# Kernel optimization log

Hardware: AMD Instinct MI355X
Metric: run time of the kernel (lower is better)

The kernel has to match this reference:

```python
import jax, jax.numpy as jnp
import numpy as np

B, N, H, DH, CZ = 1, 768, 16, 32, 128
D = H * DH  # 512
EPS = 1e-5


def layer_norm(x, w, b):
    mu = jnp.mean(x, axis=-1, keepdims=True)
    var = jnp.var(x, axis=-1, keepdims=True)
    return (x - mu) * jax.lax.rsqrt(var + EPS) * w + b


def setup_inputs() -> dict:
    key = jax.random.key(0)
    ks = jax.random.split(key, 10)
    sc = 0.02
    return {
        "s": jax.random.normal(ks[0], (B, N, D), jnp.float32),
        "z": jax.random.normal(ks[1], (B, N, N, CZ), jnp.float32),
        "norm_s_w": jnp.ones((D,), jnp.float32),
        "norm_s_b": jnp.zeros((D,), jnp.float32),
        "q_w": jax.random.normal(ks[2], (D, D), jnp.float32) * sc,
        "q_b": jax.random.normal(ks[3], (D,), jnp.float32) * sc,
        "k_w": jax.random.normal(ks[4], (D, D), jnp.float32) * sc,
        "v_w": jax.random.normal(ks[5], (D, D), jnp.float32) * sc,
        "g_w": jax.random.normal(ks[6], (D, D), jnp.float32) * sc,
        "zn_w": jnp.ones((CZ,), jnp.float32),
        "zn_b": jnp.zeros((CZ,), jnp.float32),
        "z_w": jax.random.normal(ks[7], (CZ, H), jnp.float32) * sc,
        "o_w": jax.random.normal(ks[8], (D, D), jnp.float32) * sc,
    }


def reference(s, z, norm_s_w, norm_s_b, q_w, q_b, k_w, v_w, g_w, zn_w, zn_b, z_w, o_w):
    # initial_norm on s
    s_n = layer_norm(s, norm_s_w, norm_s_b)
    # QKV projections (q has bias, k/v do not)
    q = (s_n @ q_w + q_b).reshape(B, N, H, DH)
    k = (s_n @ k_w).reshape(B, N, H, DH)
    v = (s_n @ v_w).reshape(B, N, H, DH)
    # attention scores [B, H, N, N]
    scores = jnp.einsum("bihd,bjhd->bhij", q, k) * (DH ** -0.5)
    # pair bias: layernorm(z) then linear c_z -> H, permute to [B, H, N, N]
    z_bias = layer_norm(z, zn_w, zn_b) @ z_w            # [B, N, N, H]
    z_bias = jnp.transpose(z_bias, (0, 3, 1, 2))         # [B, H, N, N]
    a = jax.nn.softmax(scores + z_bias, axis=-1)
    # attend
    o = jnp.einsum("bhij,bjhd->bihd", a, v).reshape(B, N, D)
    # sigmoid gate from normed s
    g = jax.nn.sigmoid(s_n @ g_w)
    # output projection
    return (o * g) @ o_w
```

## Files before the change

kernel.cpp:

```cpp
#include <hip/hip_runtime.h>
#include <hip/hip_bf16.h>

typedef float f32x4 __attribute__((ext_vector_type(4)));
typedef short bf16x8 __attribute__((ext_vector_type(8)));
typedef unsigned short u16;

#define NTOK 768
#define DMOD 512
#define NH   16
#define DH   32
#define CZd  128
#define NN   (768*768)

static __device__ __forceinline__ u16 f2bf(float f) {
  __hip_bfloat16 h = __float2bfloat16(f);
  return __builtin_bit_cast(u16, h);
}
static __device__ __forceinline__ float bf2f(u16 u) {
  unsigned int x = ((unsigned int)u) << 16;
  return __builtin_bit_cast(float, x);
}

__global__ __launch_bounds__(256) void prep_kernel(
    const float* __restrict__ s, const float* __restrict__ nsw, const float* __restrict__ nsb,
    const float* __restrict__ qw, const float* __restrict__ kw, const float* __restrict__ vw,
    const float* __restrict__ gw, const float* __restrict__ ow,
    const float* __restrict__ z, const float* __restrict__ znw, const float* __restrict__ znb,
    const float* __restrict__ zwp,
    u16* __restrict__ wbf, u16* __restrict__ snb, u16* __restrict__ biasb) {
  __shared__ char SM[18432];
  int bid = blockIdx.x;
  int t = threadIdx.x;

  if (bid < 1280) {
    float (*tbuf)[33] = (float(*)[33])SM;
    int seg = bid / 256;
    int tile = bid % 256;
    int k0 = (tile / 16) * 32;
    int n0 = (tile % 16) * 32;
    const float* src = seg==0?qw: seg==1?kw: seg==2?vw: seg==3?gw: ow;
    u16* out = wbf + (size_t)seg * (DMOD*DMOD);
    int tr  = t / 8;
    int tc4 = (t % 8) * 4;
    float4 v = *(const float4*)(src + (size_t)(k0+tr)*DMOD + n0 + tc4);
    tbuf[tr][tc4+0]=v.x; tbuf[tr][tc4+1]=v.y; tbuf[tr][tc4+2]=v.z; tbuf[tr][tc4+3]=v.w;
    __syncthreads();
    int nr  = t / 8;
    int kc4 = (t % 8) * 4;
    ushort4 o;
    o.x = f2bf(tbuf[kc4+0][nr]);
    o.y = f2bf(tbuf[kc4+1][nr]);
    o.z = f2bf(tbuf[kc4+2][nr]);
    o.w = f2bf(tbuf[kc4+3][nr]);
    *(ushort4*)(out + (size_t)(n0+nr)*DMOD + k0 + kc4) = o;
    return;
  }

  if (bid < 1472) {
    int i = (bid - 1280)*4 + (t >> 6);
    int lane = t & 63;
    const float* row = s + (size_t)i*DMOD + lane*8;
    float4 a0 = *(const float4*)(row);
    float4 a1 = *(const float4*)(row + 4);
    float sum = a0.x+a0.y+a0.z+a0.w + a1.x+a1.y+a1.z+a1.w;
    float sq  = a0.x*a0.x+a0.y*a0.y+a0.z*a0.z+a0.w*a0.w
              + a1.x*a1.x+a1.y*a1.y+a1.z*a1.z+a1.w*a1.w;
    #pragma unroll
    for (int mk=1; mk<64; mk<<=1) { sum += __shfl_xor(sum,mk); sq += __shfl_xor(sq,mk); }
    float mu  = sum * (1.f/512.f);
    float var = sq  * (1.f/512.f) - mu*mu;
    float rs  = rsqrtf(var + 1e-5f);
    float4 w0 = *(const float4*)(nsw + lane*8);
    float4 w1 = *(const float4*)(nsw + lane*8 + 4);
    float4 b0 = *(const float4*)(nsb + lane*8);
    float4 b1 = *(const float4*)(nsb + lane*8 + 4);
    bf16x8 o;
    o[0]=(short)f2bf((a0.x-mu)*rs*w0.x+b0.x);
    o[1]=(short)f2bf((a0.y-mu)*rs*w0.y+b0.y);
    o[2]=(short)f2bf((a0.z-mu)*rs*w0.z+b0.z);
    o[3]=(short)f2bf((a0.w-mu)*rs*w0.w+b0.w);
    o[4]=(short)f2bf((a1.x-mu)*rs*w1.x+b1.x);
    o[5]=(short)f2bf((a1.y-mu)*rs*w1.y+b1.y);
    o[6]=(short)f2bf((a1.z-mu)*rs*w1.z+b1.z);
    o[7]=(short)f2bf((a1.w-mu)*rs*w1.w+b1.w);
    *(bf16x8*)(snb + (size_t)i*DMOD + lane*8) = o;
    return;
  }

  u16*   zt   = (u16*)SM;
  float* znws = (float*)(SM + 17408);
  float* znbs = (float*)(SM + 17920);
  int zb = bid - 1472;
  int i = zb / 12, j0 = (zb % 12) * 64;
  int lane = t & 63, wv = t >> 6;
  int c16 = lane & 15, c4 = lane >> 4;
  if (t < 128) znws[t] = znw[t];
  else znbs[t-128] = znb[t-128];
  int rsub = t >> 5;
  int ch4  = (t & 31) * 4;
  const float* ztile = z + ((size_t)i*NTOK + j0)*CZd;
  float4 xv[8];
  #pragma unroll
  for (int it=0; it<8; it++)
    xv[it] = *(const float4*)(ztile + (size_t)(it*8 + rsub)*CZd + ch4);
  bf16x8 bfr[4];
  #pragma unroll
  for (int ks=0; ks<4; ks++) {
    #pragma unroll
    for (int jj=0; jj<8; jj++)
      bfr[ks][jj] = (short)f2bf(zwp[(ks*32 + c4*8 + jj)*16 + c16]);
  }
  float mu8[8], rs8[8];
  #pragma unroll
  for (int it=0; it<8; it++) {
    float4 v = xv[it];
    float sum = v.x+v.y+v.z+v.w;
    float sq  = v.x*v.x+v.y*v.y+v.z*v.z+v.w*v.w;
    #pragma unroll
    for (int mk=1; mk<32; mk<<=1) { sum += __shfl_xor(sum,mk); sq += __shfl_xor(sq,mk); }
    float mu = sum*(1.f/128.f);
    mu8[it] = mu;
    rs8[it] = rsqrtf(sq*(1.f/128.f) - mu*mu + 1e-5f);
  }
  __syncthreads();
  float4 w4 = *(const float4*)(znws + ch4);
  float4 b4 = *(const float4*)(znbs + ch4);
  #pragma unroll
  for (int it=0; it<8; it++) {
    float4 v = xv[it];
    float mu = mu8[it], rs = rs8[it];
    ushort4 o;
    o.x = f2bf((v.x-mu)*rs*w4.x + b4.x);
    o.y = f2bf((v.y-mu)*rs*w4.y + b4.y);
    o.z = f2bf((v.z-mu)*rs*w4.z + b4.z);
    o.w = f2bf((v.w-mu)*rs*w4.w + b4.w);
    *(ushort4*)(zt + (it*8 + rsub)*136 + ch4) = o;
  }
  __syncthreads();
  f32x4 acc = {0,0,0,0};
  #pragma unroll
  for (int ks=0; ks<4; ks++) {
    bf16x8 af = *(const bf16x8*)(zt + (wv*16 + c16)*136 + ks*32 + c4*8);
    acc = __builtin_amdgcn_mfma_f32_16x16x32_bf16(af, bfr[ks], acc, 0,0,0);
  }
  int jl = j0 + wv*16 + c4*4;
  u16* bp = biasb + (size_t)c16*NN + (size_t)i*NTOK + jl;
  ushort4 st;
  st.x = f2bf(acc[0]); st.y = f2bf(acc[1]); st.z = f2bf(acc[2]); st.w = f2bf(acc[3]);
  *(ushort4*)bp = st;
}

__global__ __launch_bounds__(256) void qkvg_kernel(
    const u16* __restrict__ sn, const u16* __restrict__ wts, const float* __restrict__ qb,
    u16* __restrict__ qo, u16* __restrict__ ko, u16* __restrict__ vTo, float* __restrict__ go) {
  __shared__ u16 As[32*40];
  __shared__ u16 Bs[64*40];
  int bid = blockIdx.x;
  int mb = bid % 24, nb = bid / 24;
  int wsel = nb >> 3, n0 = (nb & 7) * 64, m0 = mb * 32;
  const u16* wt = wts + (size_t)wsel * (DMOD*DMOD);
  int t = threadIdx.x, lane = t & 63, wv = t >> 6;
  int wm = (wv >> 1) * 16, wn = (wv & 1) * 32;
  int c16 = lane & 15, c4 = lane >> 4;
  int sr = t >> 2, sc = t & 3;
  f32x4 acc0={0,0,0,0}, acc1={0,0,0,0};
  for (int k0 = 0; k0 < DMOD; k0 += 32) {
    bf16x8 av;
    if (t < 128) av = *(const bf16x8*)(sn + (size_t)(m0+sr)*DMOD + k0 + sc*8);
    bf16x8 bv = *(const bf16x8*)(wt + (size_t)(n0+sr)*DMOD + k0 + sc*8);
    __syncthreads();
    if (t < 128) *(bf16x8*)(As + sr*40 + sc*8) = av;
    *(bf16x8*)(Bs + sr*40 + sc*8) = bv;
    __syncthreads();
    bf16x8 a  = *(const bf16x8*)(As + (wm + c16)*40      + c4*8);
    bf16x8 b0 = *(const bf16x8*)(Bs + (wn + c16)*40      + c4*8);
    bf16x8 b1 = *(const bf16x8*)(Bs + (wn + 16 + c16)*40 + c4*8);
    acc0 = __builtin_amdgcn_mfma_f32_16x16x32_bf16(a,b0,acc0,0,0,0);
    acc1 = __builtin_amdgcn_mfma_f32_16x16x32_bf16(a,b1,acc1,0,0,0);
  }
  int r0 = c4*4;
  #pragma unroll
  for (int bn=0; bn<2; bn++) {
    f32x4 acc = bn==0?acc0:acc1;
    #pragma unroll
    for (int rr=0; rr<4; rr++) {
      int i = m0 + wm + r0 + rr;
      int n = n0 + wn + bn*16 + c16;
      float val = acc[rr];
      if (wsel == 0)      { val += qb[n]; qo[(size_t)i*DMOD + n] = f2bf(val); }
      else if (wsel == 1) { ko[(size_t)i*DMOD + n] = f2bf(val); }
      else if (wsel == 2) { vTo[(size_t)n*NTOK + i] = f2bf(val); }
      else                { go[(size_t)i*DMOD + n] = 1.f/(1.f + expf(-val)); }
    }
  }
}

__global__ __launch_bounds__(256) void attn_kernel(
    const u16* __restrict__ qm, const u16* __restrict__ km, const u16* __restrict__ vTm,
    const u16* __restrict__ bias, const float* __restrict__ gm, u16* __restrict__ og) {
  __shared__ u16 Bt[4][16*72];
  __shared__ u16 Pt[4][16*72];
  __shared__ float OS[4][16][33];
  __shared__ float LS[4][16];
  int h  = blockIdx.x & 15;
  int i0 = (blockIdx.x >> 4) * 16;
  int t = threadIdx.x, lane = t & 63, wv = t >> 6;
  int c16 = lane & 15, c4 = lane >> 4, r0 = c4 * 4;
  bf16x8 qf = *(const bf16x8*)(qm + (size_t)(i0 + c16)*DMOD + h*DH + c4*8);
  f32x4 o0 = {0,0,0,0}, o1 = {0,0,0,0};
  float ls[4] = {0.f,0.f,0.f,0.f};
  const float scale = 0.17677669529663687f;
  const u16* bbase = bias + (size_t)h*NN + (size_t)i0*NTOK;
  int br = lane >> 3;
  int bc = (lane & 7) * 8;
  u16* bt = &Bt[wv][0];
  u16* pt = &Pt[wv][0];
  for (int jj = 0; jj < 3; jj++) {
    int j0 = wv*192 + jj*64;
    bf16x8 bv0 = *(const bf16x8*)(bbase + (size_t)br*NTOK     + j0 + bc);
    bf16x8 bv1 = *(const bf16x8*)(bbase + (size_t)(br+8)*NTOK + j0 + bc);
    bf16x8 kf0 = *(const bf16x8*)(km + (size_t)(j0 +  0 + c16)*DMOD + h*DH + c4*8);
    bf16x8 kf1 = *(const bf16x8*)(km + (size_t)(j0 + 16 + c16)*DMOD + h*DH + c4*8);
    bf16x8 kf2 = *(const bf16x8*)(km + (size_t)(j0 + 32 + c16)*DMOD + h*DH + c4*8);
    bf16x8 kf3 = *(const bf16x8*)(km + (size_t)(j0 + 48 + c16)*DMOD + h*DH + c4*8);
    *(bf16x8*)(bt + br*72 + bc)     = bv0;
    *(bf16x8*)(bt + (br+8)*72 + bc) = bv1;
    f32x4 zz = {0,0,0,0};
    f32x4 s0 = __builtin_amdgcn_mfma_f32_16x16x32_bf16(qf,kf0,zz,0,0,0);
    f32x4 s1 = __builtin_amdgcn_mfma_f32_16x16x32_bf16(qf,kf1,zz,0,0,0);
    f32x4 s2 = __builtin_amdgcn_mfma_f32_16x16x32_bf16(qf,kf2,zz,0,0,0);
    f32x4 s3 = __builtin_amdgcn_mfma_f32_16x16x32_bf16(qf,kf3,zz,0,0,0);
    #pragma unroll
    for (int rr=0; rr<4; rr++) {
      int row = (r0 + rr) * 72;
      float p0 = __expf(s0[rr]*scale + bf2f(bt[row + 0*16 + c16]));
      float p1 = __expf(s1[rr]*scale + bf2f(bt[row + 1*16 + c16]));
      float p2 = __expf(s2[rr]*scale + bf2f(bt[row + 2*16 + c16]));
      float p3 = __expf(s3[rr]*scale + bf2f(bt[row + 3*16 + c16]));
      ls[rr] += p0 + p1 + p2 + p3;
      pt[row + 0*16 + c16] = f2bf(p0);
      pt[row + 1*16 + c16] = f2bf(p1);
      pt[row + 2*16 + c16] = f2bf(p2);
      pt[row + 3*16 + c16] = f2bf(p3);
    }
    #pragma unroll
    for (int ks=0; ks<2; ks++) {
      bf16x8 pf = *(const bf16x8*)(pt + c16*72 + ks*32 + c4*8);
      bf16x8 v0 = *(const bf16x8*)(vTm + (size_t)(h*DH + c16)*NTOK      + j0 + ks*32 + c4*8);
      bf16x8 v1 = *(const bf16x8*)(vTm + (size_t)(h*DH + 16 + c16)*NTOK + j0 + ks*32 + c4*8);
      o0 = __builtin_amdgcn_mfma_f32_16x16x32_bf16(pf, v0, o0, 0,0,0);
      o1 = __builtin_amdgcn_mfma_f32_16x16x32_bf16(pf, v1, o1, 0,0,0);
    }
  }
  #pragma unroll
  for (int rr=0; rr<4; rr++) {
    float l = ls[rr];
    l += __shfl_xor(l,1); l += __shfl_xor(l,2); l += __shfl_xor(l,4); l += __shfl_xor(l,8);
    OS[wv][r0+rr][c16]      = o0[rr];
    OS[wv][r0+rr][16 + c16] = o1[rr];
    if (c16 == 0) LS[wv][r0+rr] = l;
  }
  __syncthreads();
  #pragma unroll
  for (int u=0; u<2; u++) {
    int idx = t + u*256;
    int row = idx >> 5, d = idx & 31;
    float osum = OS[0][row][d] + OS[1][row][d] + OS[2][row][d] + OS[3][row][d];
    float lsum = LS[0][row] + LS[1][row] + LS[2][row] + LS[3][row];
    int i = i0 + row;
    float g = gm[(size_t)i*DMOD + h*DH + d];
    og[(size_t)i*DMOD + h*DH + d] = f2bf(osum/lsum*g);
  }
}

__global__ __launch_bounds__(256) void out_kernel(
    const u16* __restrict__ og, const u16* __restrict__ owT, float* __restrict__ out) {
  __shared__ u16 As[32*40];
  __shared__ u16 Bs[64*40];
  int bid = blockIdx.x;
  int mb = bid % 24, nb = bid / 24;
  int m0 = mb*32, n0 = nb*64;
  int t = threadIdx.x, lane = t & 63, wv = t >> 6;
  int wm = (wv >> 1) * 16, wn = (wv & 1) * 32;
  int c16 = lane & 15, c4 = lane >> 4;
  int sr = t >> 2, sc = t & 3;
  f32x4 acc0={0,0,0,0}, acc1={0,0,0,0};
  for (int k0 = 0; k0 < DMOD; k0 += 32) {
    bf16x8 av;
    if (t < 128) av = *(const bf16x8*)(og + (size_t)(m0+sr)*DMOD + k0 + sc*8);
    bf16x8 bv = *(const bf16x8*)(owT + (size_t)(n0+sr)*DMOD + k0 + sc*8);
    __syncthreads();
    if (t < 128) *(bf16x8*)(As + sr*40 + sc*8) = av;
    *(bf16x8*)(Bs + sr*40 + sc*8) = bv;
    __syncthreads();
    bf16x8 a  = *(const bf16x8*)(As + (wm + c16)*40      + c4*8);
    bf16x8 b0 = *(const bf16x8*)(Bs + (wn + c16)*40      + c4*8);
    bf16x8 b1 = *(const bf16x8*)(Bs + (wn + 16 + c16)*40 + c4*8);
    acc0 = __builtin_amdgcn_mfma_f32_16x16x32_bf16(a,b0,acc0,0,0,0);
    acc1 = __builtin_amdgcn_mfma_f32_16x16x32_bf16(a,b1,acc1,0,0,0);
  }
  int r0 = c4*4;
  #pragma unroll
  for (int bn=0; bn<2; bn++) {
    f32x4 acc = bn==0?acc0:acc1;
    #pragma unroll
    for (int rr=0; rr<4; rr++)
      out[(size_t)(m0 + wm + r0 + rr)*DMOD + n0 + wn + bn*16 + c16] = acc[rr];
  }
}

extern "C" void kernel_launch(void* const* d_in, const int* in_sizes, int n_in,
                              void* d_out, int out_size, void* d_ws, size_t ws_size,
                              hipStream_t stream) {
  const float* s   = (const float*)d_in[0];
  const float* z   = (const float*)d_in[1];
  const float* nsw = (const float*)d_in[2];
  const float* nsb = (const float*)d_in[3];
  const float* qw  = (const float*)d_in[4];
  const float* qb  = (const float*)d_in[5];
  const float* kw  = (const float*)d_in[6];
  const float* vw  = (const float*)d_in[7];
  const float* gw  = (const float*)d_in[8];
  const float* znw = (const float*)d_in[9];
  const float* znb = (const float*)d_in[10];
  const float* zw  = (const float*)d_in[11];
  const float* ow  = (const float*)d_in[12];
  float* out = (float*)d_out;

  char* p = (char*)d_ws;
  u16* w_bf    = (u16*)p;  p += (size_t)5*DMOD*DMOD*2;
  u16* sn_bf   = (u16*)p;  p += (size_t)NTOK*DMOD*2;
  u16* q_bf    = (u16*)p;  p += (size_t)NTOK*DMOD*2;
  u16* k_bf    = (u16*)p;  p += (size_t)NTOK*DMOD*2;
  u16* vT_bf   = (u16*)p;  p += (size_t)NTOK*DMOD*2;
  float* g_f   = (float*)p; p += (size_t)NTOK*DMOD*4;
  u16* og_bf   = (u16*)p;  p += (size_t)NTOK*DMOD*2;
  u16* bias_bf = (u16*)p;  p += (size_t)NH*NN*2;

  prep_kernel<<<dim3(10688), dim3(256), 0, stream>>>(
      s, nsw, nsb, qw, kw, vw, gw, ow, z, znw, znb, zw, w_bf, sn_bf, bias_bf);
  qkvg_kernel<<<dim3(768), dim3(256), 0, stream>>>(sn_bf, w_bf, qb, q_bf, k_bf, vT_bf, g_f);
  attn_kernel<<<dim3(768), dim3(256), 0, stream>>>(q_bf, k_bf, vT_bf, bias_bf, g_f, og_bf);
  out_kernel<<<dim3(192), dim3(256), 0, stream>>>(og_bf, w_bf + (size_t)4*DMOD*DMOD, out);
}
```

Before: 101.1 us.

## Split z-bias prep kernel, relayout bias as [i,h,j], drop LDS staging in GEMMs

Splits the prep kernel in two. A small kernel pretransposes z_w to bf16, and a separate zprep kernel normalizes z with per-row 8-lane reductions and wider loads. The pair-bias buffer is reordered to [i][h][j], and the attention kernel now reads bias straight from global memory instead of staging it in LDS. The QKVG and output GEMMs drop shared-memory tiling and barriers and load MFMA fragments directly from global memory with unrolling. This trades LDS traffic and syncs for more global and L2 traffic, and adds one extra kernel launch.

```diff
diff --git a/kernel.cpp b/kernel.cpp
--- a/kernel.cpp
+++ b/kernel.cpp
@@ -21,19 +21,16 @@
   return __builtin_bit_cast(float, x);
 }
 
-__global__ __launch_bounds__(256) void prep_kernel(
+__global__ __launch_bounds__(256) void pre_kernel(
     const float* __restrict__ s, const float* __restrict__ nsw, const float* __restrict__ nsb,
     const float* __restrict__ qw, const float* __restrict__ kw, const float* __restrict__ vw,
-    const float* __restrict__ gw, const float* __restrict__ ow,
-    const float* __restrict__ z, const float* __restrict__ znw, const float* __restrict__ znb,
-    const float* __restrict__ zwp,
-    u16* __restrict__ wbf, u16* __restrict__ snb, u16* __restrict__ biasb) {
-  __shared__ char SM[18432];
+    const float* __restrict__ gw, const float* __restrict__ ow, const float* __restrict__ zwp,
+    u16* __restrict__ wbf, u16* __restrict__ snb, u16* __restrict__ zwT) {
   int bid = blockIdx.x;
   int t = threadIdx.x;
 
   if (bid < 1280) {
-    float (*tbuf)[33] = (float(*)[33])SM;
+    __shared__ float tbuf[32][33];
     int seg = bid / 256;
     int tile = bid % 256;
     int k0 = (tile / 16) * 32;
@@ -87,54 +84,73 @@
     return;
   }
 
-  u16*   zt   = (u16*)SM;
-  float* znws = (float*)(SM + 17408);
-  float* znbs = (float*)(SM + 17920);
-  int zb = bid - 1472;
-  int i = zb / 12, j0 = (zb % 12) * 64;
-  int lane = t & 63, wv = t >> 6;
+  #pragma unroll
+  for (int e=0; e<8; e++) {
+    int idx = t*8 + e;
+    int n = idx >> 7, k = idx & 127;
+    zwT[idx] = f2bf(zwp[k*16 + n]);
+  }
+}
+
+__global__ __launch_bounds__(256) void zprep_kernel(
+    const float* __restrict__ z, const float* __restrict__ znw, const float* __restrict__ znb,
+    const u16* __restrict__ zwT, u16* __restrict__ biasb) {
+  __shared__ u16 zt[64*136];
+  int bid = blockIdx.x;
+  int i = bid / 12, j0 = (bid % 12) * 64;
+  int t = threadIdx.x, lane = t & 63, wv = t >> 6;
   int c16 = lane & 15, c4 = lane >> 4;
-  if (t < 128) znws[t] = znw[t];
-  else znbs[t-128] = znb[t-128];
-  int rsub = t >> 5;
-  int ch4  = (t & 31) * 4;
+  int rsub = lane >> 3;
+  int ch0  = (lane & 7) * 16;
   const float* ztile = z + ((size_t)i*NTOK + j0)*CZd;
-  float4 xv[8];
-  #pragma unroll
-  for (int it=0; it<8; it++)
-    xv[it] = *(const float4*)(ztile + (size_t)(it*8 + rsub)*CZd + ch4);
+  float4 xv[2][4];
+  #pragma unroll
+  for (int g=0; g<2; g++) {
+    const float* rp = ztile + (size_t)(wv*16 + g*8 + rsub)*CZd + ch0;
+    xv[g][0] = *(const float4*)(rp);
+    xv[g][1] = *(const float4*)(rp+4);
+    xv[g][2] = *(const float4*)(rp+8);
+    xv[g][3] = *(const float4*)(rp+12);
+  }
   bf16x8 bfr[4];
   #pragma unroll
-  for (int ks=0; ks<4; ks++) {
-    #pragma unroll
-    for (int jj=0; jj<8; jj++)
-      bfr[ks][jj] = (short)f2bf(zwp[(ks*32 + c4*8 + jj)*16 + c16]);
-  }
-  float mu8[8], rs8[8];
-  #pragma unroll
-  for (int it=0; it<8; it++) {
-    float4 v = xv[it];
-    float sum = v.x+v.y+v.z+v.w;
-    float sq  = v.x*v.x+v.y*v.y+v.z*v.z+v.w*v.w;
-    #pragma unroll
-    for (int mk=1; mk<32; mk<<=1) { sum += __shfl_xor(sum,mk); sq += __shfl_xor(sq,mk); }
+  for (int ks=0; ks<4; ks++)
+    bfr[ks] = *(const bf16x8*)(zwT + c16*CZd + ks*32 + c4*8);
+  float4 w4[4], b4[4];
+  #pragma unroll
+  for (int q=0; q<4; q++) {
+    w4[q] = *(const float4*)(znw + ch0 + q*4);
+    b4[q] = *(const float4*)(znb + ch0 + q*4);
+  }
+  #pragma unroll
+  for (int g=0; g<2; g++) {
+    float sum=0.f, sq=0.f;
+    #pragma unroll
+    for (int q=0; q<4; q++) {
+      float4 v = xv[g][q];
+      sum += v.x+v.y+v.z+v.w;
+      sq  += v.x*v.x+v.y*v.y+v.z*v.z+v.w*v.w;
+    }
+    sum += __shfl_xor(sum,1); sq += __shfl_xor(sq,1);
+    sum += __shfl_xor(sum,2); sq += __shfl_xor(sq,2);
+    sum += __shfl_xor(sum,4); sq += __shfl_xor(sq,4);
     float mu = sum*(1.f/128.f);
-    mu8[it] = mu;
-    rs8[it] = rsqrtf(sq*(1.f/128.f) - mu*mu + 1e-5f);
-  }
-  __syncthreads();
-  float4 w4 = *(const float4*)(znws + ch4);
-  float4 b4 = *(const float4*)(znbs + ch4);
-  #pragma unroll
-  for (int it=0; it<8; it++) {
-    float4 v = xv[it];
-    float mu = mu8[it], rs = rs8[it];
-    ushort4 o;
-    o.x = f2bf((v.x-mu)*rs*w4.x + b4.x);
-    o.y = f2bf((v.y-mu)*rs*w4.y + b4.y);
-    o.z = f2bf((v.z-mu)*rs*w4.z + b4.z);
-    o.w = f2bf((v.w-mu)*rs*w4.w + b4.w);
-    *(ushort4*)(zt + (it*8 + rsub)*136 + ch4) = o;
+    float rs = rsqrtf(sq*(1.f/128.f) - mu*mu + 1e-5f);
+    int row = wv*16 + g*8 + rsub;
+    #pragma unroll
+    for (int hh=0; hh<2; hh++) {
+      bf16x8 o;
+      #pragma unroll
+      for (int q=0; q<2; q++) {
+        float4 v = xv[g][hh*2+q];
+        float4 w = w4[hh*2+q], b = b4[hh*2+q];
+        o[q*4+0]=(short)f2bf((v.x-mu)*rs*w.x+b.x);
+        o[q*4+1]=(short)f2bf((v.y-mu)*rs*w.y+b.y);
+        o[q*4+2]=(short)f2bf((v.z-mu)*rs*w.z+b.z);
+        o[q*4+3]=(short)f2bf((v.w-mu)*rs*w.w+b.w);
+      }
+      *(bf16x8*)(zt + row*136 + ch0 + hh*8) = o;
+    }
   }
   __syncthreads();
   f32x4 acc = {0,0,0,0};
@@ -144,7 +160,7 @@
     acc = __builtin_amdgcn_mfma_f32_16x16x32_bf16(af, bfr[ks], acc, 0,0,0);
   }
   int jl = j0 + wv*16 + c4*4;
-  u16* bp = biasb + (size_t)c16*NN + (size_t)i*NTOK + jl;
+  u16* bp = biasb + ((size_t)i*NH + c16)*NTOK + jl;
   ushort4 st;
   st.x = f2bf(acc[0]); st.y = f2bf(acc[1]); st.z = f2bf(acc[2]); st.w = f2bf(acc[3]);
   *(ushort4*)bp = st;
@@ -153,8 +169,6 @@
 __global__ __launch_bounds__(256) void qkvg_kernel(
     const u16* __restrict__ sn, const u16* __restrict__ wts, const float* __restrict__ qb,
     u16* __restrict__ qo, u16* __restrict__ ko, u16* __restrict__ vTo, float* __restrict__ go) {
-  __shared__ u16 As[32*40];
-  __shared__ u16 Bs[64*40];
   int bid = blockIdx.x;
   int mb = bid % 24, nb = bid / 24;
   int wsel = nb >> 3, n0 = (nb & 7) * 64, m0 = mb * 32;
@@ -162,19 +176,15 @@
   int t = threadIdx.x, lane = t & 63, wv = t >> 6;
   int wm = (wv >> 1) * 16, wn = (wv & 1) * 32;
   int c16 = lane & 15, c4 = lane >> 4;
-  int sr = t >> 2, sc = t & 3;
+  const u16* arow  = sn + (size_t)(m0 + wm + c16)*DMOD + c4*8;
+  const u16* brow0 = wt + (size_t)(n0 + wn + c16)*DMOD + c4*8;
+  const u16* brow1 = wt + (size_t)(n0 + wn + 16 + c16)*DMOD + c4*8;
   f32x4 acc0={0,0,0,0}, acc1={0,0,0,0};
+  #pragma unroll 4
   for (int k0 = 0; k0 < DMOD; k0 += 32) {
-    bf16x8 av;
-    if (t < 128) av = *(const bf16x8*)(sn + (size_t)(m0+sr)*DMOD + k0 + sc*8);
-    bf16x8 bv = *(const bf16x8*)(wt + (size_t)(n0+sr)*DMOD + k0 + sc*8);
-    __syncthreads();
-    if (t < 128) *(bf16x8*)(As + sr*40 + sc*8) = av;
-    *(bf16x8*)(Bs + sr*40 + sc*8) = bv;
-    __syncthreads();
-    bf16x8 a  = *(const bf16x8*)(As + (wm + c16)*40      + c4*8);
-    bf16x8 b0 = *(const bf16x8*)(Bs + (wn + c16)*40      + c4*8);
-    bf16x8 b1 = *(const bf16x8*)(Bs + (wn + 16 + c16)*40 + c4*8);
+    bf16x8 a  = *(const bf16x8*)(arow  + k0);
+    bf16x8 b0 = *(const bf16x8*)(brow0 + k0);
+    bf16x8 b1 = *(const bf16x8*)(brow1 + k0);
     acc0 = __builtin_amdgcn_mfma_f32_16x16x32_bf16(a,b0,acc0,0,0,0);
     acc1 = __builtin_amdgcn_mfma_f32_16x16x32_bf16(a,b1,acc1,0,0,0);
   }
@@ -198,7 +208,6 @@
 __global__ __launch_bounds__(256) void attn_kernel(
     const u16* __restrict__ qm, const u16* __restrict__ km, const u16* __restrict__ vTm,
     const u16* __restrict__ bias, const float* __restrict__ gm, u16* __restrict__ og) {
-  __shared__ u16 Bt[4][16*72];
   __shared__ u16 Pt[4][16*72];
   __shared__ float OS[4][16][33];
   __shared__ float LS[4][16];
@@ -210,21 +219,14 @@
   f32x4 o0 = {0,0,0,0}, o1 = {0,0,0,0};
   float ls[4] = {0.f,0.f,0.f,0.f};
   const float scale = 0.17677669529663687f;
-  const u16* bbase = bias + (size_t)h*NN + (size_t)i0*NTOK;
-  int br = lane >> 3;
-  int bc = (lane & 7) * 8;
-  u16* bt = &Bt[wv][0];
+  const u16* bbase = bias + ((size_t)i0*NH + h)*NTOK;
   u16* pt = &Pt[wv][0];
   for (int jj = 0; jj < 3; jj++) {
     int j0 = wv*192 + jj*64;
-    bf16x8 bv0 = *(const bf16x8*)(bbase + (size_t)br*NTOK     + j0 + bc);
-    bf16x8 bv1 = *(const bf16x8*)(bbase + (size_t)(br+8)*NTOK + j0 + bc);
     bf16x8 kf0 = *(const bf16x8*)(km + (size_t)(j0 +  0 + c16)*DMOD + h*DH + c4*8);
     bf16x8 kf1 = *(const bf16x8*)(km + (size_t)(j0 + 16 + c16)*DMOD + h*DH + c4*8);
     bf16x8 kf2 = *(const bf16x8*)(km + (size_t)(j0 + 32 + c16)*DMOD + h*DH + c4*8);
     bf16x8 kf3 = *(const bf16x8*)(km + (size_t)(j0 + 48 + c16)*DMOD + h*DH + c4*8);
-    *(bf16x8*)(bt + br*72 + bc)     = bv0;
-    *(bf16x8*)(bt + (br+8)*72 + bc) = bv1;
     f32x4 zz = {0,0,0,0};
     f32x4 s0 = __builtin_amdgcn_mfma_f32_16x16x32_bf16(qf,kf0,zz,0,0,0);
     f32x4 s1 = __builtin_amdgcn_mfma_f32_16x16x32_bf16(qf,kf1,zz,0,0,0);
@@ -232,11 +234,12 @@
     f32x4 s3 = __builtin_amdgcn_mfma_f32_16x16x32_bf16(qf,kf3,zz,0,0,0);
     #pragma unroll
     for (int rr=0; rr<4; rr++) {
+      const u16* bp = bbase + (size_t)(r0+rr)*(NH*NTOK) + j0 + c16;
       int row = (r0 + rr) * 72;
-      float p0 = __expf(s0[rr]*scale + bf2f(bt[row + 0*16 + c16]));
-      float p1 = __expf(s1[rr]*scale + bf2f(bt[row + 1*16 + c16]));
-      float p2 = __expf(s2[rr]*scale + bf2f(bt[row + 2*16 + c16]));
-      float p3 = __expf(s3[rr]*scale + bf2f(bt[row + 3*16 + c16]));
+      float p0 = __expf(s0[rr]*scale + bf2f(bp[ 0]));
+      float p1 = __expf(s1[rr]*scale + bf2f(bp[16]));
+      float p2 = __expf(s2[rr]*scale + bf2f(bp[32]));
+      float p3 = __expf(s3[rr]*scale + bf2f(bp[48]));
       ls[rr] += p0 + p1 + p2 + p3;
       pt[row + 0*16 + c16] = f2bf(p0);
       pt[row + 1*16 + c16] = f2bf(p1);
@@ -275,27 +278,21 @@
 
 __global__ __launch_bounds__(256) void out_kernel(
     const u16* __restrict__ og, const u16* __restrict__ owT, float* __restrict__ out) {
-  __shared__ u16 As[32*40];
-  __shared__ u16 Bs[64*40];
   int bid = blockIdx.x;
   int mb = bid % 24, nb = bid / 24;
   int m0 = mb*32, n0 = nb*64;
   int t = threadIdx.x, lane = t & 63, wv = t >> 6;
   int wm = (wv >> 1) * 16, wn = (wv & 1) * 32;
   int c16 = lane & 15, c4 = lane >> 4;
-  int sr = t >> 2, sc = t & 3;
+  const u16* arow  = og  + (size_t)(m0 + wm + c16)*DMOD + c4*8;
+  const u16* brow0 = owT + (size_t)(n0 + wn + c16)*DMOD + c4*8;
+  const u16* brow1 = owT + (size_t)(n0 + wn + 16 + c16)*DMOD + c4*8;
   f32x4 acc0={0,0,0,0}, acc1={0,0,0,0};
+  #pragma unroll 4
   for (int k0 = 0; k0 < DMOD; k0 += 32) {
-    bf16x8 av;
-    if (t < 128) av = *(const bf16x8*)(og + (size_t)(m0+sr)*DMOD + k0 + sc*8);
-    bf16x8 bv = *(const bf16x8*)(owT + (size_t)(n0+sr)*DMOD + k0 + sc*8);
-    __syncthreads();
-    if (t < 128) *(bf16x8*)(As + sr*40 + sc*8) = av;
-    *(bf16x8*)(Bs + sr*40 + sc*8) = bv;
-    __syncthreads();
-    bf16x8 a  = *(const bf16x8*)(As + (wm + c16)*40      + c4*8);
-    bf16x8 b0 = *(const bf16x8*)(Bs + (wn + c16)*40      + c4*8);
-    bf16x8 b1 = *(const bf16x8*)(Bs + (wn + 16 + c16)*40 + c4*8);
+    bf16x8 a  = *(const bf16x8*)(arow  + k0);
+    bf16x8 b0 = *(const bf16x8*)(brow0 + k0);
+    bf16x8 b1 = *(const bf16x8*)(brow1 + k0);
     acc0 = __builtin_amdgcn_mfma_f32_16x16x32_bf16(a,b0,acc0,0,0,0);
     acc1 = __builtin_amdgcn_mfma_f32_16x16x32_bf16(a,b1,acc1,0,0,0);
   }
@@ -336,9 +333,11 @@
   float* g_f   = (float*)p; p += (size_t)NTOK*DMOD*4;
   u16* og_bf   = (u16*)p;  p += (size_t)NTOK*DMOD*2;
   u16* bias_bf = (u16*)p;  p += (size_t)NH*NN*2;
-
-  prep_kernel<<<dim3(10688), dim3(256), 0, stream>>>(
-      s, nsw, nsb, qw, kw, vw, gw, ow, z, znw, znb, zw, w_bf, sn_bf, bias_bf);
+  u16* zwT_bf  = (u16*)p;  p += (size_t)NH*CZd*2;
+
+  pre_kernel<<<dim3(1473), dim3(256), 0, stream>>>(
+      s, nsw, nsb, qw, kw, vw, gw, ow, zw, w_bf, sn_bf, zwT_bf);
+  zprep_kernel<<<dim3(9216), dim3(256), 0, stream>>>(z, znw, znb, zwT_bf, bias_bf);
   qkvg_kernel<<<dim3(768), dim3(256), 0, stream>>>(sn_bf, w_bf, qb, q_bf, k_bf, vT_bf, g_f);
   attn_kernel<<<dim3(768), dim3(256), 0, stream>>>(q_bf, k_bf, vT_bf, bias_bf, g_f, og_bf);
   out_kernel<<<dim3(192), dim3(256), 0, stream>>>(og_bf, w_bf + (size_t)4*DMOD*DMOD, out);
```

Result: slower. 110.5 us (+9.2%).
